# Optimization experiments

Hardware: AMD Instinct MI355X
Metric: run time of the kernel (lower is better)

The kernel has to match this reference:

```python
import jax, jax.numpy as jnp
import numpy as np

N = 100000   # nodes
E = 3200000  # edges (avg degree 32)
D = 20       # state_dim
ACT = 5      # action_dim
NEG_SLOPE = 0.2  # PyG GATConv leaky_relu default


def setup_inputs() -> dict:
    key = jax.random.key(0)
    ks = jax.random.split(key, 18)
    s = 1.0 / np.sqrt(D)
    inp = {
        "x": jax.random.normal(ks[0], (N, D), jnp.float32),
        "edge_index": jax.random.randint(ks[1], (2, E), 0, N, dtype=jnp.int32),
        "edge_attr": jax.random.normal(ks[2], (E, 1), jnp.float32),
        # GCNConv params
        "gcn_W": jax.random.normal(ks[3], (D, D), jnp.float32) * s,
        "gcn_b": jnp.zeros((D,), jnp.float32),
        # GATConv params (heads=1)
        "gat_W": jax.random.normal(ks[4], (D, D), jnp.float32) * s,
        "gat_att_src": jax.random.normal(ks[5], (D,), jnp.float32) * s,
        "gat_att_dst": jax.random.normal(ks[6], (D,), jnp.float32) * s,
        "gat_b": jnp.zeros((D,), jnp.float32),
        # dueling head MLPs
        "aW1": jax.random.normal(ks[7], (D, D), jnp.float32) * s,
        "ab1": jnp.zeros((D,), jnp.float32),
        "aW2": jax.random.normal(ks[8], (D, ACT), jnp.float32) * s,
        "ab2": jnp.zeros((ACT,), jnp.float32),
        "vW1": jax.random.normal(ks[9], (D, D), jnp.float32) * s,
        "vb1": jnp.zeros((D,), jnp.float32),
        "vW2": jax.random.normal(ks[10], (D, 1), jnp.float32) * s,
        "vb2": jnp.zeros((1,), jnp.float32),
    }
    return inp


def _add_self_loops(src, dst, n):
    loop = jnp.arange(n, dtype=src.dtype)
    return jnp.concatenate([src, loop]), jnp.concatenate([dst, loop])


def _gcn_conv(x, src, dst, W, b):
    # PyG GCNConv: symmetric normalization with self loops, then scatter-add.
    h = x @ W                                           # [N, D]
    deg = jax.ops.segment_sum(jnp.ones_like(dst, jnp.float32), dst, num_segments=N)
    dinv = jnp.where(deg > 0, jax.lax.rsqrt(jnp.maximum(deg, 1e-12)), 0.0)
    norm = dinv[src] * dinv[dst]                        # [E+N]
    msg = norm[:, None] * h[src]                        # gather + scale
    return jax.ops.segment_sum(msg, dst, num_segments=N) + b


def _gat_conv(x, src, dst, W, att_src, att_dst, b):
    # PyG GATConv heads=1: per-edge attention, softmax over incoming edges.
    h = x @ W                                           # [N, D]
    a_s = h @ att_src                                   # [N]
    a_d = h @ att_dst                                   # [N]
    e = jax.nn.leaky_relu(a_s[src] + a_d[dst], NEG_SLOPE)  # [E+N]
    m = jax.ops.segment_max(e, dst, num_segments=N)     # per-dst max (stable softmax)
    ex = jnp.exp(e - m[dst])
    denom = jax.ops.segment_sum(ex, dst, num_segments=N)
    alpha = ex / denom[dst]
    out = jax.ops.segment_sum(alpha[:, None] * h[src], dst, num_segments=N)
    return out + b


def reference(x, edge_index, edge_attr, gcn_W, gcn_b, gat_W, gat_att_src,
              gat_att_dst, gat_b, aW1, ab1, aW2, ab2, vW1, vb1, vW2, vb2):
    src, dst = _add_self_loops(edge_index[0], edge_index[1], N)
    h = jax.nn.relu(_gcn_conv(x, src, dst, gcn_W, gcn_b))
    h = jax.nn.relu(_gat_conv(h, src, dst, gat_W, gat_att_src, gat_att_dst, gat_b))
    g = jnp.sum(h, axis=0, keepdims=True)               # [1, D] graph readout
    A = jax.nn.relu(g @ aW1 + ab1) @ aW2 + ab2          # [1, ACT]
    V = jax.nn.relu(g @ vW1 + vb1) @ vW2 + vb2          # [1, 1]
    Q = V + A - jnp.mean(A, axis=1, keepdims=True)      # dueling combine
    return Q
```

## Files before the change

kernel.cpp:

```cpp
#include <hip/hip_runtime.h>

#define D 20
#define ACT 5
#define NEG_SLOPE 0.2f
#define NBUK 512
#define CPAD 16
#define NSUP 13
#define SUBS 32

typedef float f32x2 __attribute__((ext_vector_type(2)));
#if defined(__has_builtin)
#if __has_builtin(__builtin_amdgcn_cvt_pk_f32_fp8) && __has_builtin(__builtin_amdgcn_cvt_pk_fp8_f32)
#define HW_FP8 1
#endif
#endif

__device__ __forceinline__ float leaky(float x) {
    return x > 0.f ? x : NEG_SLOPE * x;
}

#ifndef HW_FP8
__device__ __forceinline__ float dec1(unsigned b) {
    unsigned s = (b & 0x80u) << 24;
    unsigned em = (b & 0x7fu) << 20;
    return __uint_as_float(s | em) * __uint_as_float(0x7b800000u);
}
__device__ __forceinline__ unsigned enc1(float x) {
    x = fminf(fmaxf(x, -448.f), 448.f);
    unsigned u = __float_as_uint(x * __uint_as_float(0x03800000u));
    unsigned s = (u >> 24) & 0x80u;
    u &= 0x7fffffffu;
    u += 0x7ffffu + ((u >> 20) & 1u);
    unsigned v = (u >> 20) & 0x7fu;
    if (v > 0x7eu) v = 0x7eu;
    return s | v;
}
#endif

__device__ __forceinline__ void dec4(unsigned q, float* o) {
#ifdef HW_FP8
    f32x2 lo = __builtin_amdgcn_cvt_pk_f32_fp8((int)q, false);
    f32x2 hi = __builtin_amdgcn_cvt_pk_f32_fp8((int)q, true);
    o[0] = lo.x; o[1] = lo.y; o[2] = hi.x; o[3] = hi.y;
#else
    o[0] = dec1(q & 255u); o[1] = dec1((q >> 8) & 255u);
    o[2] = dec1((q >> 16) & 255u); o[3] = dec1(q >> 24);
#endif
}
__device__ __forceinline__ unsigned enc4(float a, float b, float c, float d) {
    a = fminf(fmaxf(a, -448.f), 448.f);
    b = fminf(fmaxf(b, -448.f), 448.f);
    c = fminf(fmaxf(c, -448.f), 448.f);
    d = fminf(fmaxf(d, -448.f), 448.f);
#ifdef HW_FP8
    int t = __builtin_amdgcn_cvt_pk_fp8_f32(a, b, 0, false);
    t = __builtin_amdgcn_cvt_pk_fp8_f32(c, d, t, true);
    return (unsigned)t;
#else
    return enc1(a) | (enc1(b) << 8) | (enc1(c) << 16) | (enc1(d) << 24);
#endif
}
__device__ __forceinline__ void dec_row(uint4 a, unsigned q4, float* v) {
    dec4(a.x, v + 0); dec4(a.y, v + 4); dec4(a.z, v + 8);
    dec4(a.w, v + 12); dec4(q4, v + 16);
}

__global__ void k_bhist(const int* __restrict__ dst, int* __restrict__ bkt, int e) {
    __shared__ int lh[NBUK];
    for (int b = threadIdx.x; b < NBUK; b += blockDim.x) lh[b] = 0;
    __syncthreads();
    int stride = gridDim.x * blockDim.x;
    int tid = blockIdx.x * blockDim.x + threadIdx.x;
    int n4 = e >> 2;
    const int4* d4 = (const int4*)dst;
    for (int i = tid; i < n4; i += stride) {
        int4 v = d4[i];
        atomicAdd(&lh[v.x >> 8], 1);
        atomicAdd(&lh[v.y >> 8], 1);
        atomicAdd(&lh[v.z >> 8], 1);
        atomicAdd(&lh[v.w >> 8], 1);
    }
    for (int i = (n4 << 2) + tid; i < e; i += stride)
        atomicAdd(&lh[dst[i] >> 8], 1);
    __syncthreads();
    for (int b = threadIdx.x; b < NBUK; b += blockDim.x) {
        int c = lh[b];
        if (c) atomicAdd(&bkt[b * CPAD], c);
    }
}

__global__ void k_bscan(const int* __restrict__ bkt, int* __restrict__ bbase,
                        int* __restrict__ bcur, int* __restrict__ scur,
                        int* __restrict__ off_n, int e) {
    __shared__ int wtot[4];
    int t = threadIdx.x;
    int c0 = bkt[(2 * t) * CPAD];
    int c1 = bkt[(2 * t + 1) * CPAD];
    int v = c0 + c1;
    int lane = t & 63, wv = t >> 6;
    int s = v;
    for (int o = 1; o < 64; o <<= 1) {
        int u = __shfl_up(s, o);
        if (lane >= o) s += u;
    }
    if (lane == 63) wtot[wv] = s;
    __syncthreads();
    int wb = 0;
    for (int k = 0; k < wv; ++k) wb += wtot[k];
    int base = wb + s - v;
    bbase[2 * t] = base;
    bbase[2 * t + 1] = base + c0;
    bcur[(2 * t) * CPAD] = base;
    bcur[(2 * t + 1) * CPAD] = base + c0;
    if ((t & 15) == 0) scur[(t >> 4) * CPAD] = base;
    if (t == 255) bbase[NBUK] = base + v;
    if (t == 0) *off_n = e;
}

__global__ void kA_bin(const int* __restrict__ src, const int* __restrict__ dst,
                       int* __restrict__ scur, unsigned* __restrict__ tmp2,
                       int e, int nba) {
    __shared__ int lh[16];
    if (threadIdx.x < 16) lh[threadIdx.x] = 0;
    __syncthreads();
    int chunk = (((e + nba - 1) / nba) + 3) & ~3;
    int lo = blockIdx.x * chunk, hi = min(lo + chunk, e);
    int cnt = hi - lo;
    int n4 = cnt > 0 ? (cnt >> 2) : 0;
    const int4* d4 = (const int4*)(dst + lo);
    for (int i = threadIdx.x; i < n4; i += blockDim.x) {
        int4 v = d4[i];
        atomicAdd(&lh[v.x >> 13], 1);
        atomicAdd(&lh[v.y >> 13], 1);
        atomicAdd(&lh[v.z >> 13], 1);
        atomicAdd(&lh[v.w >> 13], 1);
    }
    for (int j = lo + (n4 << 2) + threadIdx.x; j < hi; j += blockDim.x)
        atomicAdd(&lh[dst[j] >> 13], 1);
    __syncthreads();
    if (threadIdx.x < 16) {
        int c = lh[threadIdx.x];
        lh[threadIdx.x] = c ? atomicAdd(&scur[threadIdx.x * CPAD], c) : 0;
    }
    __syncthreads();
    const int4* s4 = (const int4*)(src + lo);
    for (int i = threadIdx.x; i < n4; i += blockDim.x) {
        int4 dv = d4[i];
        int4 sv = s4[i];
        int p;
        p = atomicAdd(&lh[dv.x >> 13], 1);
        tmp2[p] = ((unsigned)sv.x << 13) | (unsigned)(dv.x & 8191);
        p = atomicAdd(&lh[dv.y >> 13], 1);
        tmp2[p] = ((unsigned)sv.y << 13) | (unsigned)(dv.y & 8191);
        p = atomicAdd(&lh[dv.z >> 13], 1);
        tmp2[p] = ((unsigned)sv.z << 13) | (unsigned)(dv.z & 8191);
        p = atomicAdd(&lh[dv.w >> 13], 1);
        tmp2[p] = ((unsigned)sv.w << 13) | (unsigned)(dv.w & 8191);
    }
    for (int j = lo + (n4 << 2) + threadIdx.x; j < hi; j += blockDim.x) {
        int t = dst[j];
        int p = atomicAdd(&lh[t >> 13], 1);
        tmp2[p] = ((unsigned)src[j] << 13) | (unsigned)(t & 8191);
    }
}

__global__ void kB_bin(const unsigned* __restrict__ tmp2, const int* __restrict__ bbase,
                       int* __restrict__ bcur, unsigned* __restrict__ tmp) {
    __shared__ int lh[SUBS];
    int g = blockIdx.x;
    int s = g % NSUP;
    int slice = g / NSUP;
    int b0 = s * SUBS;
    int slo = bbase[b0], shi = bbase[b0 + SUBS];
    int cnt = shi - slo;
    int sl = (cnt + 31) / 32;
    int lo = slo + slice * sl, hi = min(lo + sl, shi);
    if (threadIdx.x < SUBS) lh[threadIdx.x] = 0;
    __syncthreads();
    for (int j = lo + threadIdx.x; j < hi; j += blockDim.x)
        atomicAdd(&lh[(tmp2[j] >> 8) & 31u], 1);
    __syncthreads();
    if (threadIdx.x < SUBS) {
        int c = lh[threadIdx.x];
        lh[threadIdx.x] = c ? atomicAdd(&bcur[(b0 + threadIdx.x) * CPAD], c) : 0;
    }
    __syncthreads();
    for (int j = lo + threadIdx.x; j < hi; j += blockDim.x) {
        unsigned v = tmp2[j];
        int p = atomicAdd(&lh[(v >> 8) & 31u], 1);
        tmp[p] = ((v >> 13) << 8) | (v & 255u);
    }
}

__global__ void k_bin1(const int* __restrict__ src, const int* __restrict__ dst,
                       int* __restrict__ bcur, unsigned* __restrict__ tmp,
                       int e, int nba) {
    __shared__ int lh[NBUK];
    for (int b = threadIdx.x; b < NBUK; b += blockDim.x) lh[b] = 0;
    __syncthreads();
    int chunk = (((e + nba - 1) / nba) + 3) & ~3;
    int lo = blockIdx.x * chunk, hi = min(lo + chunk, e);
    for (int j = lo + threadIdx.x; j < hi; j += blockDim.x)
        atomicAdd(&lh[dst[j] >> 8], 1);
    __syncthreads();
    for (int b = threadIdx.x; b < NBUK; b += blockDim.x) {
        int c = lh[b];
        lh[b] = c ? atomicAdd(&bcur[b * CPAD], c) : 0;
    }
    __syncthreads();
    for (int j = lo + threadIdx.x; j < hi; j += blockDim.x) {
        int t = dst[j];
        int p = atomicAdd(&lh[t >> 8], 1);
        tmp[p] = ((unsigned)src[j] << 8) | (unsigned)(t & 255);
    }
}

__global__ void k_scatter2(const unsigned* __restrict__ tmp, const int* __restrict__ bbase,
                           int* __restrict__ off, int* __restrict__ esrc, int n) {
    __shared__ int ldeg[256];
    __shared__ int lcur[256];
    __shared__ int wtot[4];
    int b = blockIdx.x;
    int t = threadIdx.x;
    int nlo = b << 8;
    int nloc = min(nlo + 256, n) - nlo;
    int lo = bbase[b], hi = bbase[b + 1];

    if (t < 256) ldeg[t] = 0;
    __syncthreads();
    for (int i = lo + t; i < hi; i += blockDim.x)
        atomicAdd(&ldeg[tmp[i] & 255u], 1);
    __syncthreads();

    if (t < 256) {
        int v = ldeg[t];
        int lane = t & 63, wv = t >> 6;
        int s = v;
        for (int o = 1; o < 64; o <<= 1) {
            int u = __shfl_up(s, o);
            if (lane >= o) s += u;
        }
        if (lane == 63) wtot[wv] = s;
        __syncthreads();
        int wb = 0;
        for (int k = 0; k < wv; ++k) wb += wtot[k];
        int pos = lo + wb + s - v;
        if (t < nloc) off[nlo + t] = pos;
        lcur[t] = pos;
    } else {
        __syncthreads();
    }
    __syncthreads();

    for (int i = lo + t; i < hi; i += blockDim.x) {
        unsigned w = tmp[i];
        int p = atomicAdd(&lcur[w & 255u], 1);
        esrc[p] = (int)(w >> 8);
    }
}

__global__ void k_xw(const float* __restrict__ x, const float* __restrict__ W,
                     const int* __restrict__ off, uint4* __restrict__ h1c, int n) {
    __shared__ float sWT[D * D];
    for (int t = threadIdx.x; t < D * D; t += blockDim.x)
        sWT[t] = W[(t % D) * D + (t / D)];
    __syncthreads();
    int i = blockIdx.x * blockDim.x + threadIdx.x;
    if (i >= n) return;
    float xi[D];
    const float4* xr = (const float4*)(x + (size_t)i * D);
#pragma unroll
    for (int q = 0; q < D / 4; ++q) {
        float4 v = xr[q];
        xi[4 * q + 0] = v.x; xi[4 * q + 1] = v.y;
        xi[4 * q + 2] = v.z; xi[4 * q + 3] = v.w;
    }
    float h[D];
#pragma unroll
    for (int d = 0; d < D; ++d) {
        const float4* wr = (const float4*)&sWT[d * D];
        float a = 0.f;
#pragma unroll
        for (int kk = 0; kk < D / 4; ++kk) {
            float4 w = wr[kk];
            a += xi[4 * kk + 0] * w.x + xi[4 * kk + 1] * w.y
               + xi[4 * kk + 2] * w.z + xi[4 * kk + 3] * w.w;
        }
        h[d] = a;
    }
    int dg = off[i + 1] - off[i];
    uint4* o = h1c + (size_t)i * 2;
    o[0] = make_uint4(enc4(h[0], h[1], h[2], h[3]), enc4(h[4], h[5], h[6], h[7]),
                      enc4(h[8], h[9], h[10], h[11]), enc4(h[12], h[13], h[14], h[15]));
    o[1] = make_uint4(enc4(h[16], h[17], h[18], h[19]),
                      __float_as_uint(rsqrtf((float)(dg + 1))), 0u, 0u);
}

__global__ void k_gcn_gat(const int* __restrict__ off, const int* __restrict__ esrc,
                          const uint4* __restrict__ h1c, const float* __restrict__ gcn_b,
                          const float* __restrict__ gat_W, const float* __restrict__ att_s,
                          const float* __restrict__ att_d, uint4* __restrict__ h2c, int n) {
    __shared__ float sWT[D * D], sb[D], sas[D], sad[D];
    __shared__ float stage[32][D];
    for (int t = threadIdx.x; t < D * D; t += blockDim.x)
        sWT[t] = gat_W[(t % D) * D + (t / D)];
    if (threadIdx.x < D) {
        sb[threadIdx.x]  = gcn_b[threadIdx.x];
        sas[threadIdx.x] = att_s[threadIdx.x];
        sad[threadIdx.x] = att_d[threadIdx.x];
    }
    __syncthreads();
    int t = threadIdx.x;
    int i = blockIdx.x * (blockDim.x >> 3) + (t >> 3);
    int q = t & 7;
    bool valid = i < n;

    float acc[D];
#pragma unroll
    for (int d = 0; d < D; ++d) acc[d] = 0.f;

    if (valid) {
        const uint4* row = h1c + (size_t)i * 2;
        uint2 r1 = *(const uint2*)(row + 1);
        float di = __uint_as_float(r1.y);
        if (q == 0) {
            float v[D];
            dec_row(row[0], r1.x, v);
            float c = di * di;
#pragma unroll
            for (int d = 0; d < D; ++d) acc[d] = c * v[d];
        }
        int s0 = off[i], s1 = off[i + 1];
        int j = s0 + q;
        bool have = j < s1;
        uint4 a_n; uint2 b_n;
        if (have) {
            const uint4* rs = h1c + (size_t)esrc[j] * 2;
            a_n = rs[0];
            b_n = *(const uint2*)(rs + 1);
        }
        while (have) {
            uint4 a = a_n; uint2 b = b_n;
            int jn = j + 8;
            bool hn = jn < s1;
            if (hn) {
                const uint4* rs = h1c + (size_t)esrc[jn] * 2;
                a_n = rs[0];
                b_n = *(const uint2*)(rs + 1);
            }
            float v[D];
            dec_row(a, b.x, v);
            float norm = di * __uint_as_float(b.y);
#pragma unroll
            for (int d = 0; d < D; ++d) acc[d] += norm * v[d];
            j = jn; have = hn;
        }
    }
#pragma unroll
    for (int d = 0; d < D; ++d) acc[d] += __shfl_xor(acc[d], 1);
#pragma unroll
    for (int d = 0; d < D; ++d) acc[d] += __shfl_xor(acc[d], 2);
#pragma unroll
    for (int d = 0; d < D; ++d) acc[d] += __shfl_xor(acc[d], 4);

    float v[D];
#pragma unroll
    for (int k = 0; k < D; ++k) {
        float tv = acc[k] + sb[k];
        v[k] = tv > 0.f ? tv : 0.f;
    }
    int nb = t >> 3;
    int d0 = (q < 4) ? 3 * q : 12 + 2 * (q - 4);
    int nd = (q < 4) ? 3 : 2;
    float as_p = 0.f, ad_p = 0.f;
#pragma unroll
    for (int r = 0; r < 3; ++r) {
        if (r < nd) {
            int d = d0 + r;
            const float4* wr = (const float4*)&sWT[d * D];
            float a = 0.f;
#pragma unroll
            for (int kk = 0; kk < D / 4; ++kk) {
                float4 w = wr[kk];
                a += v[4 * kk + 0] * w.x + v[4 * kk + 1] * w.y
                   + v[4 * kk + 2] * w.z + v[4 * kk + 3] * w.w;
            }
            stage[nb][d] = a;
            as_p += a * sas[d];
            ad_p += a * sad[d];
        }
    }
    as_p += __shfl_xor(as_p, 1); as_p += __shfl_xor(as_p, 2); as_p += __shfl_xor(as_p, 4);
    ad_p += __shfl_xor(ad_p, 1); ad_p += __shfl_xor(ad_p, 2); ad_p += __shfl_xor(ad_p, 4);
    if (valid && q == 0) {
        const float* hs = stage[nb];
        uint4* o = h2c + (size_t)i * 2;
        o[0] = make_uint4(enc4(hs[0], hs[1], hs[2], hs[3]),
                          enc4(hs[4], hs[5], hs[6], hs[7]),
                          enc4(hs[8], hs[9], hs[10], hs[11]),
                          enc4(hs[12], hs[13], hs[14], hs[15]));
        o[1] = make_uint4(enc4(hs[16], hs[17], hs[18], hs[19]),
                          __float_as_uint(as_p), __float_as_uint(ad_p), 0u);
    }
}

__global__ void k_gat_agg(const int* __restrict__ off, const int* __restrict__ esrc,
                          const uint4* __restrict__ h2c, const float* __restrict__ gat_b,
                          float* __restrict__ partials, int PB, int n) {
    __shared__ float sb[D];
    __shared__ float swave[4][D];
    if (threadIdx.x < D) sb[threadIdx.x] = gat_b[threadIdx.x];
    __syncthreads();
    int t = threadIdx.x;
    int i = blockIdx.x * (blockDim.x >> 3) + (t >> 3);
    int o = t & 7;
    bool valid = i < n;

    float m = -1e30f, den = 0.f;
    float acc[D];
#pragma unroll
    for (int d = 0; d < D; ++d) acc[d] = 0.f;

    if (valid) {
        const uint4* row = h2c + (size_t)i * 2;
        uint4 r1 = row[1];
        float ad_i = __uint_as_float(r1.z);
        if (o == 0) {
            m = leaky(__uint_as_float(r1.y) + ad_i);
            den = 1.f;
            float v[D];
            dec_row(row[0], r1.x, v);
#pragma unroll
            for (int d = 0; d < D; ++d) acc[d] = v[d];
        }
        int s0 = off[i], s1 = off[i + 1];
        int j = s0 + o;
        bool have = j < s1;
        uint4 a_n; uint2 b_n;
        if (have) {
            const uint4* rs = h2c + (size_t)esrc[j] * 2;
            a_n = rs[0];
            b_n = *(const uint2*)(rs + 1);
        }
        while (have) {
            uint4 a = a_n; uint2 b = b_n;
            int jn = j + 8;
            bool hn = jn < s1;
            if (hn) {
                const uint4* rs = h2c + (size_t)esrc[jn] * 2;
                a_n = rs[0];
                b_n = *(const uint2*)(rs + 1);
            }
            float v[D];
            dec_row(a, b.x, v);
            float eg = leaky(__uint_as_float(b.y) + ad_i);
            float nm = fmaxf(m, eg);
            float cs = __expf(m - nm), w = __expf(eg - nm);
            den = den * cs + w;
#pragma unroll
            for (int d = 0; d < D; ++d) acc[d] = acc[d] * cs + w * v[d];
            m = nm;
            j = jn; have = hn;
        }
    }
#pragma unroll
    for (int mask = 1; mask < 8; mask <<= 1) {
        float om = __shfl_xor(m, mask);
        float oden = __shfl_xor(den, mask);
        float nm = fmaxf(m, om);
        float c1 = __expf(m - nm), c2 = __expf(om - nm);
        den = den * c1 + oden * c2;
#pragma unroll
        for (int d = 0; d < D; ++d) {
            float oa = __shfl_xor(acc[d], mask);
            acc[d] = acc[d] * c1 + oa * c2;
        }
        m = nm;
    }
    float inv = den > 0.f ? 1.0f / den : 0.f;
#pragma unroll
    for (int d = 0; d < D; ++d) {
        float vv = acc[d] * inv + sb[d];
        vv = vv > 0.f ? vv : 0.f;
        if (!valid || o != 0) vv = 0.f;
        acc[d] = vv;
    }
    int wv = t >> 6, ln = t & 63;
#pragma unroll
    for (int d = 0; d < D; ++d) {
        float vv = acc[d];
        for (int s2 = 32; s2; s2 >>= 1) vv += __shfl_down(vv, s2);
        if (ln == 0) swave[wv][d] = vv;
    }
    __syncthreads();
    if (t < D) {
        float s = swave[0][t] + swave[1][t] + swave[2][t] + swave[3][t];
        partials[(size_t)t * PB + blockIdx.x] = s;
    }
}

__global__ void k_reduce(const float* __restrict__ partials, int PB, int nblk,
                         float* __restrict__ g) {
    __shared__ float swave[4];
    int d = blockIdx.x;
    int t = threadIdx.x;
    const float* p = partials + (size_t)d * PB;
    float s = 0.f;
    for (int i = t; i < nblk; i += blockDim.x) s += p[i];
    for (int s2 = 32; s2; s2 >>= 1) s += __shfl_down(s, s2);
    if ((t & 63) == 0) swave[t >> 6] = s;
    __syncthreads();
    if (t == 0) g[d] = swave[0] + swave[1] + swave[2] + swave[3];
}

__global__ void k_head(const float* __restrict__ g,
                       const float* __restrict__ aW1, const float* __restrict__ ab1,
                       const float* __restrict__ aW2, const float* __restrict__ ab2,
                       const float* __restrict__ vW1, const float* __restrict__ vb1,
                       const float* __restrict__ vW2, const float* __restrict__ vb2,
                       float* __restrict__ out) {
    __shared__ float sg[D], t1[D], t2[D], A[ACT], V, meanA;
    int t = threadIdx.x;
    if (t < D) sg[t] = g[t];
    __syncthreads();
    if (t < D) {
        float a = ab1[t], v = vb1[t];
        for (int k = 0; k < D; ++k) {
            a += sg[k] * aW1[k * D + t];
            v += sg[k] * vW1[k * D + t];
        }
        t1[t] = a > 0.f ? a : 0.f;
        t2[t] = v > 0.f ? v : 0.f;
    }
    __syncthreads();
    if (t < ACT) {
        float a = ab2[t];
        for (int d = 0; d < D; ++d) a += t1[d] * aW2[d * ACT + t];
        A[t] = a;
    }
    if (t == D) {
        float v = vb2[0];
        for (int d = 0; d < D; ++d) v += t2[d] * vW2[d];
        V = v;
    }
    __syncthreads();
    if (t == 0) {
        float s = 0.f;
        for (int j = 0; j < ACT; ++j) s += A[j];
        meanA = s / ACT;
    }
    __syncthreads();
    if (t < ACT) out[t] = V + A[t] - meanA;
}

extern "C" void kernel_launch(void* const* d_in, const int* in_sizes, int n_in,
                              void* d_out, int out_size, void* d_ws, size_t ws_size,
                              hipStream_t stream) {
    const float* x      = (const float*)d_in[0];
    const int*   ei     = (const int*)d_in[1];
    const float* gcn_W  = (const float*)d_in[3];
    const float* gcn_b  = (const float*)d_in[4];
    const float* gat_W  = (const float*)d_in[5];
    const float* att_s  = (const float*)d_in[6];
    const float* att_d  = (const float*)d_in[7];
    const float* gat_b  = (const float*)d_in[8];
    const float* aW1    = (const float*)d_in[9];
    const float* ab1    = (const float*)d_in[10];
    const float* aW2    = (const float*)d_in[11];
    const float* ab2    = (const float*)d_in[12];
    const float* vW1    = (const float*)d_in[13];
    const float* vb1    = (const float*)d_in[14];
    const float* vW2    = (const float*)d_in[15];
    const float* vb2    = (const float*)d_in[16];

    const int n = in_sizes[0] / D;
    const int e = in_sizes[1] / 2;
    const int* src = ei;
    const int* dst = ei + e;

    const int B = 256;
    const int nb_n = (n + B - 1) / B;
    const int nb_o = (n + 31) / 32;
    const int PB   = (nb_o + 63) & ~63;
    const int nbuk_used = (n + 255) >> 8;

    char* p = (char*)d_ws;
    size_t regionA = (size_t)e * 4;
    size_t hsz = (size_t)n * 64;
    if (hsz > regionA) regionA = hsz;
    uint4* h1c      = (uint4*)p;
    uint4* h2c      = h1c + (size_t)n * 2;
    unsigned* tmp2  = (unsigned*)p;
    p += regionA;
    float* g        = (float*)p;        p += 32 * sizeof(float);
    float* partials = (float*)p;        p += (size_t)D * PB * sizeof(float);
    int*   off      = (int*)p;          p += (size_t)(n + 1) * sizeof(int);
    int*   bkt      = (int*)p;          p += (size_t)NBUK * CPAD * sizeof(int);
    int*   bbase    = (int*)p;          p += (size_t)(NBUK + 1) * sizeof(int);
    int*   bcur     = (int*)p;          p += (size_t)NBUK * CPAD * sizeof(int);
    int*   scur     = (int*)p;          p += (size_t)16 * CPAD * sizeof(int);
    int*   esrc     = (int*)p;          p += (size_t)e * sizeof(int);
    unsigned* tmp   = (unsigned*)p;     p += (size_t)e * sizeof(unsigned);
    size_t need2 = (size_t)(p - (char*)d_ws);
    bool two_pass = ws_size >= need2;

    hipMemsetAsync(bkt, 0, NBUK * CPAD * sizeof(int), stream);

    k_bhist<<<1024, B, 0, stream>>>(dst, bkt, e);
    k_bscan<<<1, 256, 0, stream>>>(bkt, bbase, bcur, scur, &off[n], e);
    if (two_pass) {
        kA_bin<<<256, B, 0, stream>>>(src, dst, scur, tmp2, e, 256);
        kB_bin<<<NSUP * 32, B, 0, stream>>>(tmp2, bbase, bcur, tmp);
    } else {
        tmp = tmp2;
        k_bin1<<<1024, B, 0, stream>>>(src, dst, bcur, tmp, e, 1024);
    }
    k_scatter2<<<nbuk_used, 512, 0, stream>>>(tmp, bbase, off, esrc, n);
    k_xw<<<nb_n, B, 0, stream>>>(x, gcn_W, off, h1c, n);
    k_gcn_gat<<<nb_o, B, 0, stream>>>(off, esrc, h1c, gcn_b, gat_W,
                                      att_s, att_d, h2c, n);
    k_gat_agg<<<nb_o, B, 0, stream>>>(off, esrc, h2c, gat_b, partials, PB, n);
    k_reduce<<<D, B, 0, stream>>>(partials, PB, nb_o, g);
    k_head<<<1, 64, 0, stream>>>(g, aW1, ab1, aW2, ab2, vW1, vb1, vW2, vb2,
                                 (float*)d_out);
}
```

Measured before the change: 194.8 us.

## Precompute per-block bin offsets, unroll gathers 4-deep, simplify GAT online softmax

The histogram kernel now also records per-block superbucket counts, and the scan kernel turns them into deterministic per-block base offsets. The binning pass no longer needs its own histogram pass or global atomics, and its grid grows to 1024 blocks. The GCN and GAT aggregation loops now issue four independent row gathers per iteration instead of one-deep prefetching, to raise memory-level parallelism. The GAT online softmax skips rescaling unless the new logit exceeds the running max by more than 8, and the cross-lane merge is reduced to a max followed by plain sums. The cost is a more serial scan kernel (16 rounds over 1024 blocks) and more registers in the aggregation kernels.

```diff
diff --git a/kernel.cpp b/kernel.cpp
--- a/kernel.cpp
+++ b/kernel.cpp
@@ -7,6 +7,7 @@
 #define CPAD 16
 #define NSUP 13
 #define SUBS 32
+#define NBA2 1024
 
 typedef float f32x2 __attribute__((ext_vector_type(2)));
 #if defined(__has_builtin)
@@ -65,84 +66,122 @@
     dec4(a.w, v + 12); dec4(q4, v + 16);
 }
 
-__global__ void k_bhist(const int* __restrict__ dst, int* __restrict__ bkt, int e) {
+__device__ __forceinline__ void gat_upd(uint4 a, uint2 b, float ad_i,
+                                        float& m, float& den, float* acc) {
+    float v[D];
+    dec_row(a, b.x, v);
+    float eg = leaky(__uint_as_float(b.y) + ad_i);
+    if (eg <= m + 8.0f) {
+        float w = __expf(eg - m);
+        den += w;
+#pragma unroll
+        for (int d = 0; d < D; ++d) acc[d] += w * v[d];
+    } else {
+        float cs = __expf(m - eg);
+        den = den * cs + 1.0f;
+#pragma unroll
+        for (int d = 0; d < D; ++d) acc[d] = acc[d] * cs + v[d];
+        m = eg;
+    }
+}
+
+__global__ void k_bhist(const int* __restrict__ dst, int* __restrict__ bkt,
+                        int* __restrict__ blkSup, int e) {
     __shared__ int lh[NBUK];
     for (int b = threadIdx.x; b < NBUK; b += blockDim.x) lh[b] = 0;
     __syncthreads();
-    int stride = gridDim.x * blockDim.x;
-    int tid = blockIdx.x * blockDim.x + threadIdx.x;
-    int n4 = e >> 2;
-    const int4* d4 = (const int4*)dst;
-    for (int i = tid; i < n4; i += stride) {
-        int4 v = d4[i];
-        atomicAdd(&lh[v.x >> 8], 1);
-        atomicAdd(&lh[v.y >> 8], 1);
-        atomicAdd(&lh[v.z >> 8], 1);
-        atomicAdd(&lh[v.w >> 8], 1);
-    }
-    for (int i = (n4 << 2) + tid; i < e; i += stride)
-        atomicAdd(&lh[dst[i] >> 8], 1);
-    __syncthreads();
-    for (int b = threadIdx.x; b < NBUK; b += blockDim.x) {
-        int c = lh[b];
-        if (c) atomicAdd(&bkt[b * CPAD], c);
-    }
-}
-
-__global__ void k_bscan(const int* __restrict__ bkt, int* __restrict__ bbase,
-                        int* __restrict__ bcur, int* __restrict__ scur,
-                        int* __restrict__ off_n, int e) {
-    __shared__ int wtot[4];
-    int t = threadIdx.x;
-    int c0 = bkt[(2 * t) * CPAD];
-    int c1 = bkt[(2 * t + 1) * CPAD];
-    int v = c0 + c1;
-    int lane = t & 63, wv = t >> 6;
-    int s = v;
-    for (int o = 1; o < 64; o <<= 1) {
-        int u = __shfl_up(s, o);
-        if (lane >= o) s += u;
-    }
-    if (lane == 63) wtot[wv] = s;
-    __syncthreads();
-    int wb = 0;
-    for (int k = 0; k < wv; ++k) wb += wtot[k];
-    int base = wb + s - v;
-    bbase[2 * t] = base;
-    bbase[2 * t + 1] = base + c0;
-    bcur[(2 * t) * CPAD] = base;
-    bcur[(2 * t + 1) * CPAD] = base + c0;
-    if ((t & 15) == 0) scur[(t >> 4) * CPAD] = base;
-    if (t == 255) bbase[NBUK] = base + v;
-    if (t == 0) *off_n = e;
-}
-
-__global__ void kA_bin(const int* __restrict__ src, const int* __restrict__ dst,
-                       int* __restrict__ scur, unsigned* __restrict__ tmp2,
-                       int e, int nba) {
-    __shared__ int lh[16];
-    if (threadIdx.x < 16) lh[threadIdx.x] = 0;
-    __syncthreads();
-    int chunk = (((e + nba - 1) / nba) + 3) & ~3;
+    int chunk = (((e + NBA2 - 1) / NBA2) + 3) & ~3;
     int lo = blockIdx.x * chunk, hi = min(lo + chunk, e);
     int cnt = hi - lo;
     int n4 = cnt > 0 ? (cnt >> 2) : 0;
     const int4* d4 = (const int4*)(dst + lo);
     for (int i = threadIdx.x; i < n4; i += blockDim.x) {
         int4 v = d4[i];
-        atomicAdd(&lh[v.x >> 13], 1);
-        atomicAdd(&lh[v.y >> 13], 1);
-        atomicAdd(&lh[v.z >> 13], 1);
-        atomicAdd(&lh[v.w >> 13], 1);
+        atomicAdd(&lh[v.x >> 8], 1);
+        atomicAdd(&lh[v.y >> 8], 1);
+        atomicAdd(&lh[v.z >> 8], 1);
+        atomicAdd(&lh[v.w >> 8], 1);
     }
     for (int j = lo + (n4 << 2) + threadIdx.x; j < hi; j += blockDim.x)
-        atomicAdd(&lh[dst[j] >> 13], 1);
-    __syncthreads();
+        atomicAdd(&lh[dst[j] >> 8], 1);
+    __syncthreads();
+    for (int b = threadIdx.x; b < NBUK; b += blockDim.x) {
+        int c = lh[b];
+        if (c) atomicAdd(&bkt[b * CPAD], c);
+    }
     if (threadIdx.x < 16) {
-        int c = lh[threadIdx.x];
-        lh[threadIdx.x] = c ? atomicAdd(&scur[threadIdx.x * CPAD], c) : 0;
-    }
-    __syncthreads();
+        int s = threadIdx.x;
+        int tot = 0;
+#pragma unroll
+        for (int k = 0; k < SUBS; ++k) tot += lh[s * SUBS + k];
+        blkSup[blockIdx.x * 16 + s] = tot;
+    }
+}
+
+__global__ void k_bscan(const int* __restrict__ bkt, int* __restrict__ bbase,
+                        int* __restrict__ bcur, const int* __restrict__ blkSup,
+                        int* __restrict__ blkBase, int* __restrict__ off_n, int e) {
+    __shared__ int wtot[4];
+    __shared__ int ssup[16];
+    int t = threadIdx.x;
+    int lane = t & 63, wv = t >> 6;
+    {
+        int c0 = bkt[(2 * t) * CPAD];
+        int c1 = bkt[(2 * t + 1) * CPAD];
+        int v = c0 + c1;
+        int s = v;
+        for (int o = 1; o < 64; o <<= 1) {
+            int u = __shfl_up(s, o);
+            if (lane >= o) s += u;
+        }
+        if (lane == 63) wtot[wv] = s;
+        __syncthreads();
+        int wb = 0;
+        for (int k = 0; k < wv; ++k) wb += wtot[k];
+        int base = wb + s - v;
+        bbase[2 * t] = base;
+        bbase[2 * t + 1] = base + c0;
+        bcur[(2 * t) * CPAD] = base;
+        bcur[(2 * t + 1) * CPAD] = base + c0;
+        if (((2 * t) & 31) == 0) ssup[(2 * t) >> 5] = base;
+        if (t == 255) bbase[NBUK] = base + v;
+        if (t == 0) *off_n = e;
+    }
+    for (int s = 0; s < 16; ++s) {
+        __syncthreads();
+        int c0 = blkSup[(4 * t + 0) * 16 + s];
+        int c1 = blkSup[(4 * t + 1) * 16 + s];
+        int c2 = blkSup[(4 * t + 2) * 16 + s];
+        int c3 = blkSup[(4 * t + 3) * 16 + s];
+        int v = c0 + c1 + c2 + c3;
+        int sc = v;
+        for (int o = 1; o < 64; o <<= 1) {
+            int u = __shfl_up(sc, o);
+            if (lane >= o) sc += u;
+        }
+        if (lane == 63) wtot[wv] = sc;
+        __syncthreads();
+        int wb = 0;
+        for (int k = 0; k < wv; ++k) wb += wtot[k];
+        int base = ssup[s] + wb + sc - v;
+        blkBase[(4 * t + 0) * 16 + s] = base;
+        blkBase[(4 * t + 1) * 16 + s] = base + c0;
+        blkBase[(4 * t + 2) * 16 + s] = base + c0 + c1;
+        blkBase[(4 * t + 3) * 16 + s] = base + c0 + c1 + c2;
+    }
+}
+
+__global__ void kA_bin(const int* __restrict__ src, const int* __restrict__ dst,
+                       const int* __restrict__ blkBase, unsigned* __restrict__ tmp2,
+                       int e) {
+    __shared__ int lh[16];
+    if (threadIdx.x < 16) lh[threadIdx.x] = blkBase[blockIdx.x * 16 + threadIdx.x];
+    __syncthreads();
+    int chunk = (((e + NBA2 - 1) / NBA2) + 3) & ~3;
+    int lo = blockIdx.x * chunk, hi = min(lo + chunk, e);
+    int cnt = hi - lo;
+    int n4 = cnt > 0 ? (cnt >> 2) : 0;
+    const int4* d4 = (const int4*)(dst + lo);
     const int4* s4 = (const int4*)(src + lo);
     for (int i = threadIdx.x; i < n4; i += blockDim.x) {
         int4 dv = d4[i];
@@ -331,29 +370,45 @@
             for (int d = 0; d < D; ++d) acc[d] = c * v[d];
         }
         int s0 = off[i], s1 = off[i + 1];
-        int j = s0 + q;
-        bool have = j < s1;
-        uint4 a_n; uint2 b_n;
-        if (have) {
-            const uint4* rs = h1c + (size_t)esrc[j] * 2;
-            a_n = rs[0];
-            b_n = *(const uint2*)(rs + 1);
-        }
-        while (have) {
-            uint4 a = a_n; uint2 b = b_n;
-            int jn = j + 8;
-            bool hn = jn < s1;
-            if (hn) {
-                const uint4* rs = h1c + (size_t)esrc[jn] * 2;
-                a_n = rs[0];
-                b_n = *(const uint2*)(rs + 1);
+        for (int jb = s0 + q; jb < s1; jb += 32) {
+            int j1 = jb + 8, j2 = jb + 16, j3 = jb + 24;
+            bool hb = j1 < s1, hc = j2 < s1, hd = j3 < s1;
+            int e0 = esrc[jb];
+            int e1 = esrc[hb ? j1 : jb];
+            int e2 = esrc[hc ? j2 : jb];
+            int e3 = esrc[hd ? j3 : jb];
+            const uint4* r0 = h1c + (size_t)e0 * 2;
+            const uint4* r1p = h1c + (size_t)e1 * 2;
+            const uint4* r2 = h1c + (size_t)e2 * 2;
+            const uint4* r3 = h1c + (size_t)e3 * 2;
+            uint4 A0 = r0[0];  uint2 B0 = *(const uint2*)(r0 + 1);
+            uint4 A1 = r1p[0]; uint2 B1 = *(const uint2*)(r1p + 1);
+            uint4 A2 = r2[0];  uint2 B2 = *(const uint2*)(r2 + 1);
+            uint4 A3 = r3[0];  uint2 B3 = *(const uint2*)(r3 + 1);
+            {
+                float v[D]; dec_row(A0, B0.x, v);
+                float nm = di * __uint_as_float(B0.y);
+#pragma unroll
+                for (int d = 0; d < D; ++d) acc[d] += nm * v[d];
             }
-            float v[D];
-            dec_row(a, b.x, v);
-            float norm = di * __uint_as_float(b.y);
-#pragma unroll
-            for (int d = 0; d < D; ++d) acc[d] += norm * v[d];
-            j = jn; have = hn;
+            if (hb) {
+                float v[D]; dec_row(A1, B1.x, v);
+                float nm = di * __uint_as_float(B1.y);
+#pragma unroll
+                for (int d = 0; d < D; ++d) acc[d] += nm * v[d];
+            }
+            if (hc) {
+                float v[D]; dec_row(A2, B2.x, v);
+                float nm = di * __uint_as_float(B2.y);
+#pragma unroll
+                for (int d = 0; d < D; ++d) acc[d] += nm * v[d];
+            }
+            if (hd) {
+                float v[D]; dec_row(A3, B3.x, v);
+                float nm = di * __uint_as_float(B3.y);
+#pragma unroll
+                for (int d = 0; d < D; ++d) acc[d] += nm * v[d];
+            }
         }
     }
 #pragma unroll
@@ -428,54 +483,43 @@
         if (o == 0) {
             m = leaky(__uint_as_float(r1.y) + ad_i);
             den = 1.f;
-            float v[D];
-            dec_row(row[0], r1.x, v);
-#pragma unroll
-            for (int d = 0; d < D; ++d) acc[d] = v[d];
+            dec_row(row[0], r1.x, acc);
         }
         int s0 = off[i], s1 = off[i + 1];
-        int j = s0 + o;
-        bool have = j < s1;
-        uint4 a_n; uint2 b_n;
-        if (have) {
-            const uint4* rs = h2c + (size_t)esrc[j] * 2;
-            a_n = rs[0];
-            b_n = *(const uint2*)(rs + 1);
-        }
-        while (have) {
-            uint4 a = a_n; uint2 b = b_n;
-            int jn = j + 8;
-            bool hn = jn < s1;
-            if (hn) {
-                const uint4* rs = h2c + (size_t)esrc[jn] * 2;
-                a_n = rs[0];
-                b_n = *(const uint2*)(rs + 1);
-            }
-            float v[D];
-            dec_row(a, b.x, v);
-            float eg = leaky(__uint_as_float(b.y) + ad_i);
-            float nm = fmaxf(m, eg);
-            float cs = __expf(m - nm), w = __expf(eg - nm);
-            den = den * cs + w;
-#pragma unroll
-            for (int d = 0; d < D; ++d) acc[d] = acc[d] * cs + w * v[d];
-            m = nm;
-            j = jn; have = hn;
-        }
-    }
+        for (int jb = s0 + o; jb < s1; jb += 32) {
+            int j1 = jb + 8, j2 = jb + 16, j3 = jb + 24;
+            bool hb = j1 < s1, hc = j2 < s1, hd = j3 < s1;
+            int e0 = esrc[jb];
+            int e1 = esrc[hb ? j1 : jb];
+            int e2 = esrc[hc ? j2 : jb];
+            int e3 = esrc[hd ? j3 : jb];
+            const uint4* r0 = h2c + (size_t)e0 * 2;
+            const uint4* r1p = h2c + (size_t)e1 * 2;
+            const uint4* r2 = h2c + (size_t)e2 * 2;
+            const uint4* r3 = h2c + (size_t)e3 * 2;
+            uint4 A0 = r0[0];  uint2 B0 = *(const uint2*)(r0 + 1);
+            uint4 A1 = r1p[0]; uint2 B1 = *(const uint2*)(r1p + 1);
+            uint4 A2 = r2[0];  uint2 B2 = *(const uint2*)(r2 + 1);
+            uint4 A3 = r3[0];  uint2 B3 = *(const uint2*)(r3 + 1);
+            gat_upd(A0, B0, ad_i, m, den, acc);
+            if (hb) gat_upd(A1, B1, ad_i, m, den, acc);
+            if (hc) gat_upd(A2, B2, ad_i, m, den, acc);
+            if (hd) gat_upd(A3, B3, ad_i, m, den, acc);
+        }
+    }
+    float mm = m;
+    mm = fmaxf(mm, __shfl_xor(mm, 1));
+    mm = fmaxf(mm, __shfl_xor(mm, 2));
+    mm = fmaxf(mm, __shfl_xor(mm, 4));
+    float sc = __expf(m - mm);
+    den *= sc;
+#pragma unroll
+    for (int d = 0; d < D; ++d) acc[d] *= sc;
 #pragma unroll
     for (int mask = 1; mask < 8; mask <<= 1) {
-        float om = __shfl_xor(m, mask);
-        float oden = __shfl_xor(den, mask);
-        float nm = fmaxf(m, om);
-        float c1 = __expf(m - nm), c2 = __expf(om - nm);
-        den = den * c1 + oden * c2;
-#pragma unroll
-        for (int d = 0; d < D; ++d) {
-            float oa = __shfl_xor(acc[d], mask);
-            acc[d] = acc[d] * c1 + oa * c2;
-        }
-        m = nm;
+        den += __shfl_xor(den, mask);
+#pragma unroll
+        for (int d = 0; d < D; ++d) acc[d] += __shfl_xor(acc[d], mask);
     }
     float inv = den > 0.f ? 1.0f / den : 0.f;
 #pragma unroll
@@ -598,7 +642,8 @@
     int*   bkt      = (int*)p;          p += (size_t)NBUK * CPAD * sizeof(int);
     int*   bbase    = (int*)p;          p += (size_t)(NBUK + 1) * sizeof(int);
     int*   bcur     = (int*)p;          p += (size_t)NBUK * CPAD * sizeof(int);
-    int*   scur     = (int*)p;          p += (size_t)16 * CPAD * sizeof(int);
+    int*   blkSup   = (int*)p;          p += (size_t)NBA2 * 16 * sizeof(int);
+    int*   blkBase  = (int*)p;          p += (size_t)NBA2 * 16 * sizeof(int);
     int*   esrc     = (int*)p;          p += (size_t)e * sizeof(int);
     unsigned* tmp   = (unsigned*)p;     p += (size_t)e * sizeof(unsigned);
     size_t need2 = (size_t)(p - (char*)d_ws);
@@ -606,10 +651,10 @@
 
     hipMemsetAsync(bkt, 0, NBUK * CPAD * sizeof(int), stream);
 
-    k_bhist<<<1024, B, 0, stream>>>(dst, bkt, e);
-    k_bscan<<<1, 256, 0, stream>>>(bkt, bbase, bcur, scur, &off[n], e);
+    k_bhist<<<NBA2, B, 0, stream>>>(dst, bkt, blkSup, e);
+    k_bscan<<<1, 256, 0, stream>>>(bkt, bbase, bcur, blkSup, blkBase, &off[n], e);
     if (two_pass) {
-        kA_bin<<<256, B, 0, stream>>>(src, dst, scur, tmp2, e, 256);
+        kA_bin<<<NBA2, B, 0, stream>>>(src, dst, blkBase, tmp2, e);
         kB_bin<<<NSUP * 32, B, 0, stream>>>(tmp2, bbase, bcur, tmp);
     } else {
         tmp = tmp2;
```

Result: slower. 201.7 us (+3.5%).
